# Kernel optimization log

Hardware: AMD Instinct MI355X
Metric: run time of the kernel (lower is better)

## Reference

```python
import jax, jax.numpy as jnp
import numpy as np

NUM_EXPERTS = 64
TOP_K = 2
NOISE_EPS = 0.01


def setup_inputs() -> dict:
    key = jax.random.key(0)
    k1, k2, k3, k4 = jax.random.split(key, 4)
    B, D, E = 32768, 2048, NUM_EXPERTS
    x = jax.random.normal(k1, (B, D), dtype=jnp.float32)
    # original inits these to zero; use small random weights for a non-degenerate top-k
    w_gate = jax.random.normal(k2, (D, E), dtype=jnp.float32) * 0.02
    w_noise = jax.random.normal(k3, (D, E), dtype=jnp.float32) * 0.02
    noise = jax.random.normal(k4, (B, E), dtype=jnp.float32)  # tf.random.normal draw, fixed
    return {"x": x, "w_gate": w_gate, "w_noise": w_noise, "noise": noise}


def reference(x, w_gate, w_noise, noise):
    # routing_pooling='flatten' on a 2D input is identity
    pooled = x  # [B, D]
    routing = pooled @ w_gate  # [B, E]
    # noisy routing (training=True path)
    noise_stddev = jax.nn.softplus(pooled @ w_noise) + NOISE_EPS
    routing = routing + noise * noise_stddev
    # softmax_top_k: take top k+1, keep top k, softmax, scatter back to E experts
    kk = min(TOP_K + 1, NUM_EXPERTS)
    top_vals, top_idx = jax.lax.top_k(routing, kk)
    top_k_vals = top_vals[:, :TOP_K]            # [B, k]
    top_k_idx = top_idx[:, :TOP_K]              # [B, k]
    top_k_gates = jax.nn.softmax(top_k_vals, axis=-1)
    B = routing.shape[0]
    rows = jnp.arange(B)[:, None]
    # rowwise_unsorted_segment_sum -> scatter gates into expert slots
    out = jnp.zeros((B, NUM_EXPERTS), dtype=routing.dtype).at[rows, top_k_idx].add(top_k_gates)
    return out
```

## Files before the change

### kernel.cpp

```cpp
#include <hip/hip_runtime.h>
#include <math.h>


typedef _Float16 half8v __attribute__((ext_vector_type(8)));
typedef float f32x16 __attribute__((ext_vector_type(16)));

constexpr int DIMK = 2048;
constexpr int NEXP = 64;
constexpr int BM   = 128;
constexpr int BK   = 64;
constexpr int NST  = DIMK / BK;

__device__ __forceinline__ void async_load16(const void* g, void* l) {
    __builtin_amdgcn_global_load_lds(
        (const __attribute__((address_space(1))) unsigned int*)g,
        (__attribute__((address_space(3))) unsigned int*)l, 16, 0, 0);
}

__device__ __forceinline__ bool gt_pair(float a, int ia, float b, int ib) {
    return (a > b) || (a == b && ia < ib);
}

__global__ __launch_bounds__(256)
void presplit_kernel(const float* __restrict__ wg, const float* __restrict__ wn,
                     _Float16* __restrict__ wsB)
{
    int gid  = blockIdx.x * 256 + threadIdx.x;
    int lane = gid & 63;
    int fb   = gid >> 6;
    int nt   = fb & 3;
    int p    = (fb >> 2) & 1;
    int kh   = (fb >> 3) & 1;
    int c    = fb >> 4;
    const float* src = (nt < 2) ? (wg + nt * 32 + (lane & 31))
                                : (wn + (nt - 2) * 32 + (lane & 31));
    int kb = c * 32 + kh * 16 + ((lane >> 5) << 3);
    half8v hp;
    #pragma unroll
    for (int j = 0; j < 8; ++j) {
        float w = src[(size_t)(kb + j) * NEXP] * 65536.0f;
        _Float16 a = (_Float16)w;
        hp[j] = p ? (_Float16)(w - (float)a) : a;
    }
    *(half8v*)(wsB + (size_t)fb * 512 + lane * 8) = hp;
}

__global__ __launch_bounds__(1024, 4)
void routing_mfma(const float* __restrict__ x, const _Float16* __restrict__ wsB,
                  const float* __restrict__ noise, float* __restrict__ out)
{
    __shared__ __align__(16) char smem[131072];
    _Float16* Bs = (_Float16*)smem;
    float*    Xs = (float*)(smem + 65536);

    const int tid  = threadIdx.x;
    const int lane = tid & 63;
    const int w    = tid >> 6;
    const int rg   = w >> 2;
    const int t    = (w >> 1) & 1;
    const int ks   = w & 1;
    const int m    = lane & 31;
    const int h    = lane >> 5;
    const int row0 = blockIdx.x * BM;

    f32x16 acc0 = {}, acc1 = {};

    const int lr0 = (w * 2 + 0) * 4 + (lane >> 4);
    const int lr1 = (w * 2 + 1) * 4 + (lane >> 4);
    const int ss0 = (lane & 15) ^ (lr0 & 15);
    const int ss1 = (lane & 15) ^ (lr1 & 15);
    const float* xsrc0 = x + (size_t)(row0 + lr0) * DIMK + ss0 * 4;
    const float* xsrc1 = x + (size_t)(row0 + lr1) * DIMK + ss1 * 4;

    auto stage = [&](int s, int buf) {
        #pragma unroll
        for (int i = 0; i < 2; ++i) {
            int j = w * 2 + i;
            async_load16(wsB + ((size_t)s * 32 + j) * 512 + lane * 8,
                         Bs + buf * 16384 + j * 512);
        }
        async_load16(xsrc0 + s * BK, Xs + buf * 8192 + (w * 2 + 0) * 256);
        async_load16(xsrc1 + s * BK, Xs + buf * 8192 + (w * 2 + 1) * 256);
    };

    stage(0, 0);
    stage(1, 1);
    __syncthreads();

    const int r    = rg * 32 + m;
    const int rx15 = r & 15;

    for (int s = 0; s < NST; ++s) {
        const int buf = s & 1;
        const float* xrow = Xs + buf * 8192 + r * 64;

        #pragma unroll
        for (int u = 0; u < 2; ++u) {
            const _Float16* bb = Bs + buf * 16384 + u * 8192
                               + (ks * 8) * 512 + lane * 8;

            half8v bH0 = *(const half8v*)(bb + (t    ) * 512);
            half8v bH1 = *(const half8v*)(bb + (2 + t) * 512);
            half8v bL0 = *(const half8v*)(bb + (4 + t    ) * 512);
            half8v bL1 = *(const half8v*)(bb + (4 + 2 + t) * 512);

            float4 x0 = *(const float4*)(xrow + ((u * 8 + ks * 4 + h * 2 + 0) ^ rx15) * 4);
            float4 x1 = *(const float4*)(xrow + ((u * 8 + ks * 4 + h * 2 + 1) ^ rx15) * 4);

            half8v aH, aL;
            {
                float f[8] = {x0.x, x0.y, x0.z, x0.w, x1.x, x1.y, x1.z, x1.w};
                #pragma unroll
                for (int j = 0; j < 8; ++j) {
                    float v = f[j] * 1024.f;
                    _Float16 a = (_Float16)v;
                    aH[j] = a; aL[j] = (_Float16)(v - (float)a);
                }
            }

            acc0 = __builtin_amdgcn_mfma_f32_32x32x16_f16(aH, bH0, acc0, 0, 0, 0);
            acc0 = __builtin_amdgcn_mfma_f32_32x32x16_f16(aH, bL0, acc0, 0, 0, 0);
            acc0 = __builtin_amdgcn_mfma_f32_32x32x16_f16(aL, bH0, acc0, 0, 0, 0);
            acc1 = __builtin_amdgcn_mfma_f32_32x32x16_f16(aH, bH1, acc1, 0, 0, 0);
            acc1 = __builtin_amdgcn_mfma_f32_32x32x16_f16(aH, bL1, acc1, 0, 0, 0);
            acc1 = __builtin_amdgcn_mfma_f32_32x32x16_f16(aL, bH1, acc1, 0, 0, 0);
        }

        __syncthreads();
        if (s + 2 < NST) stage(s + 2, buf);
    }

    const float sc = 0x1p-26f;
    constexpr int SLD = 68;
    float* scr = (float*)smem;
    {
        const int colb = t * 32 + m;
        if (ks == 0) {
            #pragma unroll
            for (int reg = 0; reg < 16; ++reg) {
                int rl = (reg & 3) + 8 * (reg >> 2) + 4 * h;
                scr[(rg * 32 + rl) * SLD + colb]            = acc0[reg] * sc;
                scr[BM * SLD + (rg * 32 + rl) * SLD + colb] = acc1[reg] * sc;
            }
        }
        __syncthreads();
        if (ks == 1) {
            #pragma unroll
            for (int reg = 0; reg < 16; ++reg) {
                int rl = (reg & 3) + 8 * (reg >> 2) + 4 * h;
                int ig = (rg * 32 + rl) * SLD + colb;
                int in = BM * SLD + ig;
                scr[ig] += acc0[reg] * sc;
                scr[in] += acc1[reg] * sc;
            }
        }
        __syncthreads();
    }

    {
        int rr = tid >> 3;
        int s8 = tid & 7;
        const float* gp = scr + rr * SLD + s8 * 8;
        const float* np = scr + BM * SLD + rr * SLD + s8 * 8;
        float4 g0 = *(const float4*)(gp);
        float4 g1 = *(const float4*)(gp + 4);
        float4 n0 = *(const float4*)(np);
        float4 n1 = *(const float4*)(np + 4);
        float4 z0 = *(const float4*)(noise + (size_t)(row0 + rr) * NEXP + s8 * 8);
        float4 z1 = *(const float4*)(noise + (size_t)(row0 + rr) * NEXP + s8 * 8 + 4);
        float gg[8] = {g0.x, g0.y, g0.z, g0.w, g1.x, g1.y, g1.z, g1.w};
        float nn[8] = {n0.x, n0.y, n0.z, n0.w, n1.x, n1.y, n1.z, n1.w};
        float zz[8] = {z0.x, z0.y, z0.z, z0.w, z1.x, z1.y, z1.z, z1.w};
        float v1 = -INFINITY, v2 = -INFINITY;
        int   i1 = 0x7ffffffe,  i2 = 0x7fffffff;
        #pragma unroll
        for (int j = 0; j < 8; ++j) {
            float nv = nn[j];
            float sp = fmaxf(nv, 0.f) + log1pf(expf(-fabsf(nv)));
            float vv = gg[j] + zz[j] * (sp + 0.01f);
            int   e  = s8 * 8 + j;
            if (gt_pair(vv, e, v1, i1)) { v2 = v1; i2 = i1; v1 = vv; i1 = e; }
            else if (gt_pair(vv, e, v2, i2)) { v2 = vv; i2 = e; }
        }
        #pragma unroll
        for (int mm = 1; mm <= 4; mm <<= 1) {
            float b1 = __shfl_xor(v1, mm); int ib1 = __shfl_xor(i1, mm);
            float b2 = __shfl_xor(v2, mm); int ib2 = __shfl_xor(i2, mm);
            if (gt_pair(b1, ib1, v1, i1)) {
                float o1 = v1; int oi1 = i1;
                v1 = b1; i1 = ib1;
                if (gt_pair(b2, ib2, o1, oi1)) { v2 = b2; i2 = ib2; }
                else                           { v2 = o1; i2 = oi1; }
            } else if (gt_pair(b1, ib1, v2, i2)) {
                v2 = b1; i2 = ib1;
            }
        }
        float te = expf(v2 - v1);
        float ga = 1.f / (1.f + te);
        float gb = te * ga;
        float* op = out + (size_t)(row0 + rr) * NEXP + s8 * 8;
        #pragma unroll
        for (int qq = 0; qq < 2; ++qq) {
            int e0 = s8 * 8 + qq * 4;
            float4 o;
            o.x = (e0 + 0 == i1) ? ga : ((e0 + 0 == i2) ? gb : 0.f);
            o.y = (e0 + 1 == i1) ? ga : ((e0 + 1 == i2) ? gb : 0.f);
            o.z = (e0 + 2 == i1) ? ga : ((e0 + 2 == i2) ? gb : 0.f);
            o.w = (e0 + 3 == i1) ? ga : ((e0 + 3 == i2) ? gb : 0.f);
            *(float4*)(op + qq * 4) = o;
        }
    }
}

extern "C" void kernel_launch(void* const* d_in, const int* in_sizes, int n_in,
                              void* d_out, int out_size, void* d_ws, size_t ws_size,
                              hipStream_t stream) {
    const float* x     = (const float*)d_in[0];
    const float* wg    = (const float*)d_in[1];
    const float* wn    = (const float*)d_in[2];
    const float* noise = (const float*)d_in[3];
    float* out = (float*)d_out;
    _Float16* wsB = (_Float16*)d_ws;

    presplit_kernel<<<dim3(256), 256, 0, stream>>>(wg, wn, wsB);

    const int Brows = in_sizes[0] / DIMK;
    dim3 grid(Brows / BM);
    routing_mfma<<<grid, 1024, 0, stream>>>(x, wsB, noise, out);
}
```

Measured before the change: 398.1 us.

## Shrink routing tile to 32 rows with 256-thread blocks and K chunks of 32

Retiles the fused gating GEMM so each block handles 32 rows with 4 waves, stepping through K in chunks of 32 instead of 128-row, 16-wave blocks with chunks of 64. Shared memory drops from 128KB to 40KB per block. The aim is to let several blocks stay resident per CU, so independent work can hide load and barrier latency. In exchange, each block re-streams the full split weight matrix, which quadruples weight traffic from L2, and each block runs twice as many loop iterations and barriers.

```diff
diff --git a/kernel.cpp b/kernel.cpp
--- a/kernel.cpp
+++ b/kernel.cpp
@@ -7,9 +7,8 @@
 
 constexpr int DIMK = 2048;
 constexpr int NEXP = 64;
-constexpr int BM   = 128;
-constexpr int BK   = 64;
-constexpr int NST  = DIMK / BK;
+constexpr int BM   = 32;
+constexpr int NCH  = DIMK / 32;
 
 __device__ __forceinline__ void async_load16(const void* g, void* l) {
     __builtin_amdgcn_global_load_lds(
@@ -45,18 +44,17 @@
     *(half8v*)(wsB + (size_t)fb * 512 + lane * 8) = hp;
 }
 
-__global__ __launch_bounds__(1024, 4)
+__global__ __launch_bounds__(256, 4)
 void routing_mfma(const float* __restrict__ x, const _Float16* __restrict__ wsB,
                   const float* __restrict__ noise, float* __restrict__ out)
 {
-    __shared__ __align__(16) char smem[131072];
+    __shared__ __align__(16) char smem[40960];
     _Float16* Bs = (_Float16*)smem;
-    float*    Xs = (float*)(smem + 65536);
+    float*    Xs = (float*)(smem + 32768);
 
     const int tid  = threadIdx.x;
     const int lane = tid & 63;
     const int w    = tid >> 6;
-    const int rg   = w >> 2;
     const int t    = (w >> 1) & 1;
     const int ks   = w & 1;
     const int m    = lane & 31;
@@ -65,69 +63,59 @@
 
     f32x16 acc0 = {}, acc1 = {};
 
-    const int lr0 = (w * 2 + 0) * 4 + (lane >> 4);
-    const int lr1 = (w * 2 + 1) * 4 + (lane >> 4);
-    const int ss0 = (lane & 15) ^ (lr0 & 15);
-    const int ss1 = (lane & 15) ^ (lr1 & 15);
-    const float* xsrc0 = x + (size_t)(row0 + lr0) * DIMK + ss0 * 4;
-    const float* xsrc1 = x + (size_t)(row0 + lr1) * DIMK + ss1 * 4;
+    const int lr  = lane >> 3;
+    const int ssx = (lane & 7) ^ (lr & 7);
+    const float* xsrc = x + (size_t)(row0 + w * 8 + lr) * DIMK + ssx * 4;
 
     auto stage = [&](int s, int buf) {
         #pragma unroll
-        for (int i = 0; i < 2; ++i) {
-            int j = w * 2 + i;
-            async_load16(wsB + ((size_t)s * 32 + j) * 512 + lane * 8,
-                         Bs + buf * 16384 + j * 512);
-        }
-        async_load16(xsrc0 + s * BK, Xs + buf * 8192 + (w * 2 + 0) * 256);
-        async_load16(xsrc1 + s * BK, Xs + buf * 8192 + (w * 2 + 1) * 256);
+        for (int i = 0; i < 4; ++i) {
+            int j = w * 4 + i;
+            async_load16(wsB + ((size_t)s * 16 + j) * 512 + lane * 8,
+                         Bs + buf * 8192 + j * 512);
+        }
+        async_load16(xsrc + s * 32, Xs + buf * 1024 + w * 256);
     };
 
     stage(0, 0);
     stage(1, 1);
     __syncthreads();
 
-    const int r    = rg * 32 + m;
-    const int rx15 = r & 15;
-
-    for (int s = 0; s < NST; ++s) {
+    const int rx7 = m & 7;
+
+    for (int s = 0; s < NCH; ++s) {
         const int buf = s & 1;
-        const float* xrow = Xs + buf * 8192 + r * 64;
-
-        #pragma unroll
-        for (int u = 0; u < 2; ++u) {
-            const _Float16* bb = Bs + buf * 16384 + u * 8192
-                               + (ks * 8) * 512 + lane * 8;
-
-            half8v bH0 = *(const half8v*)(bb + (t    ) * 512);
-            half8v bH1 = *(const half8v*)(bb + (2 + t) * 512);
-            half8v bL0 = *(const half8v*)(bb + (4 + t    ) * 512);
-            half8v bL1 = *(const half8v*)(bb + (4 + 2 + t) * 512);
-
-            float4 x0 = *(const float4*)(xrow + ((u * 8 + ks * 4 + h * 2 + 0) ^ rx15) * 4);
-            float4 x1 = *(const float4*)(xrow + ((u * 8 + ks * 4 + h * 2 + 1) ^ rx15) * 4);
-
-            half8v aH, aL;
-            {
-                float f[8] = {x0.x, x0.y, x0.z, x0.w, x1.x, x1.y, x1.z, x1.w};
-                #pragma unroll
-                for (int j = 0; j < 8; ++j) {
-                    float v = f[j] * 1024.f;
-                    _Float16 a = (_Float16)v;
-                    aH[j] = a; aL[j] = (_Float16)(v - (float)a);
-                }
-            }
-
-            acc0 = __builtin_amdgcn_mfma_f32_32x32x16_f16(aH, bH0, acc0, 0, 0, 0);
-            acc0 = __builtin_amdgcn_mfma_f32_32x32x16_f16(aH, bL0, acc0, 0, 0, 0);
-            acc0 = __builtin_amdgcn_mfma_f32_32x32x16_f16(aL, bH0, acc0, 0, 0, 0);
-            acc1 = __builtin_amdgcn_mfma_f32_32x32x16_f16(aH, bH1, acc1, 0, 0, 0);
-            acc1 = __builtin_amdgcn_mfma_f32_32x32x16_f16(aH, bL1, acc1, 0, 0, 0);
-            acc1 = __builtin_amdgcn_mfma_f32_32x32x16_f16(aL, bH1, acc1, 0, 0, 0);
-        }
+        const float*    xrow = Xs + buf * 1024 + m * 32;
+        const _Float16* bb   = Bs + buf * 8192 + (ks * 8) * 512 + lane * 8;
+
+        half8v bH0 = *(const half8v*)(bb + (t    ) * 512);
+        half8v bH1 = *(const half8v*)(bb + (2 + t) * 512);
+        half8v bL0 = *(const half8v*)(bb + (4 + t    ) * 512);
+        half8v bL1 = *(const half8v*)(bb + (4 + 2 + t) * 512);
+
+        float4 x0 = *(const float4*)(xrow + ((ks * 4 + h * 2 + 0) ^ rx7) * 4);
+        float4 x1 = *(const float4*)(xrow + ((ks * 4 + h * 2 + 1) ^ rx7) * 4);
+
+        half8v aH, aL;
+        {
+            float f[8] = {x0.x, x0.y, x0.z, x0.w, x1.x, x1.y, x1.z, x1.w};
+            #pragma unroll
+            for (int j = 0; j < 8; ++j) {
+                float v = f[j] * 1024.f;
+                _Float16 a = (_Float16)v;
+                aH[j] = a; aL[j] = (_Float16)(v - (float)a);
+            }
+        }
+
+        acc0 = __builtin_amdgcn_mfma_f32_32x32x16_f16(aH, bH0, acc0, 0, 0, 0);
+        acc0 = __builtin_amdgcn_mfma_f32_32x32x16_f16(aH, bL0, acc0, 0, 0, 0);
+        acc0 = __builtin_amdgcn_mfma_f32_32x32x16_f16(aL, bH0, acc0, 0, 0, 0);
+        acc1 = __builtin_amdgcn_mfma_f32_32x32x16_f16(aH, bH1, acc1, 0, 0, 0);
+        acc1 = __builtin_amdgcn_mfma_f32_32x32x16_f16(aH, bL1, acc1, 0, 0, 0);
+        acc1 = __builtin_amdgcn_mfma_f32_32x32x16_f16(aL, bH1, acc1, 0, 0, 0);
 
         __syncthreads();
-        if (s + 2 < NST) stage(s + 2, buf);
+        if (s + 2 < NCH) stage(s + 2, buf);
     }
 
     const float sc = 0x1p-26f;
@@ -139,8 +127,8 @@
             #pragma unroll
             for (int reg = 0; reg < 16; ++reg) {
                 int rl = (reg & 3) + 8 * (reg >> 2) + 4 * h;
-                scr[(rg * 32 + rl) * SLD + colb]            = acc0[reg] * sc;
-                scr[BM * SLD + (rg * 32 + rl) * SLD + colb] = acc1[reg] * sc;
+                scr[rl * SLD + colb]            = acc0[reg] * sc;
+                scr[BM * SLD + rl * SLD + colb] = acc1[reg] * sc;
             }
         }
         __syncthreads();
@@ -148,7 +136,7 @@
             #pragma unroll
             for (int reg = 0; reg < 16; ++reg) {
                 int rl = (reg & 3) + 8 * (reg >> 2) + 4 * h;
-                int ig = (rg * 32 + rl) * SLD + colb;
+                int ig = rl * SLD + colb;
                 int in = BM * SLD + ig;
                 scr[ig] += acc0[reg] * sc;
                 scr[in] += acc1[reg] * sc;
@@ -226,5 +214,5 @@
 
     const int Brows = in_sizes[0] / DIMK;
     dim3 grid(Brows / BM);
-    routing_mfma<<<grid, 1024, 0, stream>>>(x, wsB, noise, out);
-}
+    routing_mfma<<<grid, 256, 0, stream>>>(x, wsB, noise, out);
+}
```

Measured after the change: 406.2 us. 2.0% more time.

## Read split weights from global memory and stage only x tiles in LDS

Applied to the files above, without the earlier changes.

The B operand (pre-split fp16 weights) is no longer staged through shared memory; each wave loads its fragments directly from global memory, relying on the cache since the weights are small and shared by all blocks. The whole LDS buffer now holds larger x tiles (64 rows by 256 K, double-buffered) with an XOR swizzle over 64 chunks. The block shrinks to 512 threads and 64 rows, so there are twice as many blocks and four times fewer K stages and barriers. The cost is global-load latency on the weight fragments inside the MFMA loop, and the 128 KB LDS allocation still limits how many blocks fit on a CU.

```diff
diff --git a/kernel.cpp b/kernel.cpp
--- a/kernel.cpp
+++ b/kernel.cpp
@@ -7,8 +7,8 @@
 
 constexpr int DIMK = 2048;
 constexpr int NEXP = 64;
-constexpr int BM   = 128;
-constexpr int BK   = 64;
+constexpr int BM   = 64;
+constexpr int BK   = 256;
 constexpr int NST  = DIMK / BK;
 
 __device__ __forceinline__ void async_load16(const void* g, void* l) {
@@ -45,13 +45,12 @@
     *(half8v*)(wsB + (size_t)fb * 512 + lane * 8) = hp;
 }
 
-__global__ __launch_bounds__(1024, 4)
+__global__ __launch_bounds__(512, 2)
 void routing_mfma(const float* __restrict__ x, const _Float16* __restrict__ wsB,
                   const float* __restrict__ noise, float* __restrict__ out)
 {
     __shared__ __align__(16) char smem[131072];
-    _Float16* Bs = (_Float16*)smem;
-    float*    Xs = (float*)(smem + 65536);
+    float* Xs = (float*)smem;
 
     const int tid  = threadIdx.x;
     const int lane = tid & 63;
@@ -65,47 +64,39 @@
 
     f32x16 acc0 = {}, acc1 = {};
 
-    const int lr0 = (w * 2 + 0) * 4 + (lane >> 4);
-    const int lr1 = (w * 2 + 1) * 4 + (lane >> 4);
-    const int ss0 = (lane & 15) ^ (lr0 & 15);
-    const int ss1 = (lane & 15) ^ (lr1 & 15);
-    const float* xsrc0 = x + (size_t)(row0 + lr0) * DIMK + ss0 * 4;
-    const float* xsrc1 = x + (size_t)(row0 + lr1) * DIMK + ss1 * 4;
-
     auto stage = [&](int s, int buf) {
         #pragma unroll
-        for (int i = 0; i < 2; ++i) {
-            int j = w * 2 + i;
-            async_load16(wsB + ((size_t)s * 32 + j) * 512 + lane * 8,
-                         Bs + buf * 16384 + j * 512);
-        }
-        async_load16(xsrc0 + s * BK, Xs + buf * 8192 + (w * 2 + 0) * 256);
-        async_load16(xsrc1 + s * BK, Xs + buf * 8192 + (w * 2 + 1) * 256);
+        for (int i = 0; i < 8; ++i) {
+            int r = w * 8 + i;
+            const float* g = x + (size_t)(row0 + r) * DIMK + s * BK
+                           + ((lane ^ (r & 63)) << 2);
+            async_load16(g, Xs + buf * 16384 + r * 256);
+        }
     };
 
     stage(0, 0);
     stage(1, 1);
     __syncthreads();
 
-    const int r    = rg * 32 + m;
-    const int rx15 = r & 15;
+    const int r  = rg * 32 + m;
+    const int rk = r & 63;
 
     for (int s = 0; s < NST; ++s) {
         const int buf = s & 1;
-        const float* xrow = Xs + buf * 8192 + r * 64;
-
-        #pragma unroll
-        for (int u = 0; u < 2; ++u) {
-            const _Float16* bb = Bs + buf * 16384 + u * 8192
-                               + (ks * 8) * 512 + lane * 8;
-
-            half8v bH0 = *(const half8v*)(bb + (t    ) * 512);
-            half8v bH1 = *(const half8v*)(bb + (2 + t) * 512);
+        const float* xrow = Xs + buf * 16384 + r * 256;
+
+        #pragma unroll
+        for (int u = 0; u < 8; ++u) {
+            const int c = s * 8 + u;
+            const _Float16* bb = wsB + ((size_t)c * 16 + ks * 8) * 512 + lane * 8;
+
+            half8v bH0 = *(const half8v*)(bb + (t        ) * 512);
+            half8v bH1 = *(const half8v*)(bb + (2 + t    ) * 512);
             half8v bL0 = *(const half8v*)(bb + (4 + t    ) * 512);
             half8v bL1 = *(const half8v*)(bb + (4 + 2 + t) * 512);
 
-            float4 x0 = *(const float4*)(xrow + ((u * 8 + ks * 4 + h * 2 + 0) ^ rx15) * 4);
-            float4 x1 = *(const float4*)(xrow + ((u * 8 + ks * 4 + h * 2 + 1) ^ rx15) * 4);
+            float4 x0 = *(const float4*)(xrow + ((u * 8 + ks * 4 + h * 2 + 0) ^ rk) * 4);
+            float4 x1 = *(const float4*)(xrow + ((u * 8 + ks * 4 + h * 2 + 1) ^ rk) * 4);
 
             half8v aH, aL;
             {
@@ -226,5 +217,5 @@
 
     const int Brows = in_sizes[0] / DIMK;
     dim3 grid(Brows / BM);
-    routing_mfma<<<grid, 1024, 0, stream>>>(x, wsB, noise, out);
-}
+    routing_mfma<<<grid, 512, 0, stream>>>(x, wsB, noise, out);
+}
```

Measured after the change: 427.6 us. +7.4%, slower.
